# Performance work log

Hardware: AMD Instinct MI355X
Metric: run time of the kernel (lower is better)

The kernel has to match this reference:

```python
import jax, jax.numpy as jnp
import numpy as np

NUM_HEADS = 12

def get_rel_pos(q_size, k_size, rel_pos):
    # q_size == k_size here; relative index = i - j + (k_size - 1)
    idx = jnp.arange(q_size)[:, None] - jnp.arange(k_size)[None, :] + (k_size - 1)
    return rel_pos[idx]  # (q_size, k_size, head_dim)


def setup_inputs() -> dict:
    key = jax.random.key(0)
    ks = jax.random.split(key, 7)
    B, H, W, C = 1, 64, 64, 768
    return {
        "x": jax.random.normal(ks[0], (B, H, W, C), jnp.float32),
        "w_qkv": jax.random.normal(ks[1], (C, 3 * C), jnp.float32) * 0.02,
        "b_qkv": jnp.zeros((3 * C,), jnp.float32),
        "w_o": jax.random.normal(ks[2], (C, C), jnp.float32) * 0.02,
        "b_o": jnp.zeros((C,), jnp.float32),
        "rel_pos_h": jax.random.normal(ks[3], (2 * H - 1, C // NUM_HEADS), jnp.float32) * 0.02,
        "rel_pos_w": jax.random.normal(ks[4], (2 * W - 1, C // NUM_HEADS), jnp.float32) * 0.02,
    }


def reference(x, w_qkv, b_qkv, w_o, b_o, rel_pos_h, rel_pos_w):
    B, H, W, C = x.shape
    NH = NUM_HEADS
    HD = C // NH
    scale = HD ** -0.5  # 0.125

    qkv = x @ w_qkv + b_qkv                                   # (B,H,W,3C)
    qkv = qkv.reshape(B, H * W, 3, NH, HD)
    qkv = jnp.transpose(qkv, (2, 0, 3, 1, 4)).reshape(3, B * NH, H * W, HD)
    q, k, v = qkv[0], qkv[1], qkv[2]                          # (B*NH, HW, HD)

    Rh = get_rel_pos(H, H, rel_pos_h)                         # (H,H,HD)
    Rw = get_rel_pos(W, W, rel_pos_w)                         # (W,W,HD)
    qr = q.reshape(B * NH, H, W, HD)
    rel_h = jnp.einsum('bhwc,hkc->bhwk', qr, Rh)              # (B*NH,H,W,H)
    rel_w = jnp.einsum('bhwc,wkc->bhwk', qr, Rw)              # (B*NH,H,W,W)

    attn = jnp.einsum('bmd,bnd->bmn', q, k) * scale           # (B*NH,HW,HW)
    attn = attn.reshape(B * NH, H, W, H, W)
    attn = attn + rel_h[:, :, :, :, None] + rel_w[:, :, :, None, :]
    attn = attn.reshape(B * NH, H * W, H * W)

    p = jax.nn.softmax(attn, axis=-1)
    o = jnp.einsum('bmn,bnd->bmd', p, v)                      # (B*NH,HW,HD)
    o = o.reshape(B, NH, H * W, HD)
    o = jnp.transpose(o, (0, 2, 1, 3)).reshape(B, H, W, C)    # heads concat in channel dim
    return o @ w_o + b_o
```

## Files before the change

kernel.cpp:

```cpp
#include <hip/hip_runtime.h>

#define DEVI __device__ __forceinline__
typedef unsigned short u16;
typedef unsigned int u32;
typedef __attribute__((ext_vector_type(4))) float f4v;
typedef __attribute__((ext_vector_type(8))) short bf8v;
typedef __attribute__((ext_vector_type(4))) u32  u32x4;
typedef __attribute__((ext_vector_type(2))) u32  u32x2;
typedef __attribute__((ext_vector_type(4))) u16  u16x4;

#define AS1 __attribute__((address_space(1)))
#define AS3 __attribute__((address_space(3)))

DEVI u16 f2bf(float x){ union{float f;u32 u;} c{x}; u32 r=(c.u+0x7FFFu+((c.u>>16)&1u))>>16; return (u16)r; }
DEVI float bf2f(u16 b){ union{u32 u;float f;} c{(u32)b<<16}; return c.f; }
DEVI f4v mfma32(bf8v a, bf8v b, f4v c){ return __builtin_amdgcn_mfma_f32_16x16x32_bf16(a,b,c,0,0,0); }
DEVI unsigned lds_off(const void* p){ return (unsigned)(unsigned long)(AS3 const void*)p; }
DEVI void glds16(const void* g, void* l){
  __builtin_amdgcn_global_load_lds((AS1 void*)g, (AS3 void*)l, 16, 0, 0);
}

static constexpr int NH = 12, HW = 4096, D = 64, C = 768;
static constexpr float LOG2E = 1.44269504f;

__global__ void qa_convx(const float* __restrict__ x, u16* __restrict__ xb, int n4){
  int i = blockIdx.x*256 + threadIdx.x;
  if(i >= n4) return;
  f4v v = ((const f4v*)x)[i];
  u16x4 o; for(int j=0;j<4;j++) o[j] = f2bf(v[j]);
  ((u16x4*)xb)[i] = o;
}

__global__ void qa_transp(const float* __restrict__ in, u16* __restrict__ out, int R, int Cc, int scale_k){
  __shared__ float tl[32][33];
  int t = threadIdx.x;
  int r0 = blockIdx.y*32, c0 = blockIdx.x*32;
  int tr = t>>3, tc = (t&7)*4;
  f4v v = *(const f4v*)&in[(r0+tr)*Cc + c0 + tc];
  for(int j=0;j<4;j++) tl[tr][tc+j] = v[j];
  __syncthreads();
  int oc = t>>3, orr = (t&7)*4;
  float sc = (scale_k && (c0+oc) >= 768 && (c0+oc) < 1536) ? 0.125f*LOG2E : 1.0f;
  u16x4 o; for(int j=0;j<4;j++) o[j] = f2bf(tl[orr+j][oc]*sc);
  *(u16x4*)&out[(c0+oc)*R + r0 + orr] = o;
}

__global__ __launch_bounds__(256,2) void qa_gemm_qkv(
    const u16* __restrict__ A, const u16* __restrict__ Bt, const float* __restrict__ bias,
    u16* __restrict__ qb, u16* __restrict__ kb, u16* __restrict__ vb){
  __shared__ u16 Al[128*32], Bl[128*32];
  const int t = threadIdx.x, lane = t&63, w = t>>6, c16 = lane&15, h4 = lane>>4;
  const int m0 = blockIdx.y*128, n0 = blockIdx.x*128;
  const int wr = w>>1, wc = w&1;
  f4v acc[4][4];
  for(int nt=0;nt<4;nt++){
    f4v bv;
    for(int r=0;r<4;r++){
      int col = n0 + wc*64 + nt*16 + 4*h4 + r;
      float b = bias[col];
      bv[r] = (col >= 768 && col < 1536) ? b*0.125f*LOG2E : b;
    }
    for(int mt=0;mt<4;mt++) acc[mt][nt] = bv;
  }
  for(int k0 = 0; k0 < 768; k0 += 32){
    __syncthreads();
    for(int i=0;i<2;i++){
      int off = i*4096 + w*1024 + lane*16;
      int row = off>>6, kk = (off&63)>>1;
      glds16(A  + (size_t)(m0+row)*768 + k0 + kk, (u16*)Al + i*2048 + w*512);
      glds16(Bt + (size_t)(n0+row)*768 + k0 + kk, (u16*)Bl + i*2048 + w*512);
    }
    __syncthreads();
    bf8v a[4], b[4];
    for(int mt=0;mt<4;mt++) a[mt] = *(const bf8v*)&Al[(wr*64+mt*16+c16)*32 + h4*8];
    for(int nt=0;nt<4;nt++) b[nt] = *(const bf8v*)&Bl[(wc*64+nt*16+c16)*32 + h4*8];
    for(int mt=0;mt<4;mt++) for(int nt=0;nt<4;nt++) acc[mt][nt] = mfma32(b[nt], a[mt], acc[mt][nt]);
  }
  for(int mt=0;mt<4;mt++){
    int row = m0 + wr*64 + mt*16 + c16;
    for(int nt=0;nt<4;nt++){
      int col0 = n0 + wc*64 + nt*16 + 4*h4;
      int which = col0/768, head = (col0>>6)%12, d0 = col0&63;
      u16* dst = which==0 ? qb : (which==1 ? kb : vb);
      u32x2 pk;
      asm("v_cvt_pk_bf16_f32 %0, %1, %2" : "=v"(pk[0]) : "v"(acc[mt][nt][0]), "v"(acc[mt][nt][1]));
      asm("v_cvt_pk_bf16_f32 %0, %1, %2" : "=v"(pk[1]) : "v"(acc[mt][nt][2]), "v"(acc[mt][nt][3]));
      *(u32x2*)&dst[((size_t)(head<<12)+row)*64 + d0] = pk;
    }
  }
}

__global__ __launch_bounds__(256) void qa_rel(
    const u16* __restrict__ qbuf, const float* __restrict__ rph, const float* __restrict__ rpw,
    u16* __restrict__ RHt, u16* __restrict__ RW){
  const int t = threadIdx.x, lane = t&63, w = t>>6, c16 = lane&15, h4 = lane>>4;
  const int qh = blockIdx.x, head = blockIdx.y;
  __shared__ u16 ql[64*72], hl[64*72], wl[128*72];
  {
    int row = t>>2, d0 = (t&3)*16;
    const u16* src = qbuf + ((size_t)(head<<12)+(qh<<6)+row)*64 + d0;
    *(u32x4*)&ql[row*72+d0]   = *(const u32x4*)src;
    *(u32x4*)&ql[row*72+d0+8] = *(const u32x4*)(src+8);
    for(int j=0;j<16;j++) hl[row*72+d0+j] = f2bf(rph[(qh+row)*64 + d0 + j]);
    int rw_r = t>>1, rd0 = (t&1)*32;
    for(int j=0;j<32;j++) wl[rw_r*72+rd0+j] = (rw_r<127) ? f2bf(rpw[rw_r*64+rd0+j]) : (u16)0;
  }
  __syncthreads();
  if(w < 2){
    bf8v a[2][2]; f4v acc[2][4] = {};
    for(int mt=0;mt<2;mt++) for(int ch=0;ch<2;ch++)
      a[mt][ch] = *(const bf8v*)&ql[(w*32+mt*16+c16)*72 + ch*32 + h4*8];
    for(int nt=0;nt<4;nt++) for(int ch=0;ch<2;ch++){
      bf8v b = *(const bf8v*)&hl[(nt*16+c16)*72 + ch*32 + h4*8];
      for(int mt=0;mt<2;mt++) acc[mt][nt] = mfma32(a[mt][ch], b, acc[mt][nt]);
    }
    for(int mt=0;mt<2;mt++) for(int nt=0;nt<4;nt++) for(int r=0;r<4;r++){
      int qw = w*32+mt*16+4*h4+r, c = nt*16+c16, kh = 63 - c;
      RHt[((size_t)(head*64+qh)*64+kh)*64 + qw] = f2bf(acc[mt][nt][r]*LOG2E);
    }
  } else {
    bf8v a[2][2]; f4v acc[2][8] = {};
    for(int mt=0;mt<2;mt++) for(int ch=0;ch<2;ch++)
      a[mt][ch] = *(const bf8v*)&ql[((w-2)*32+mt*16+c16)*72 + ch*32 + h4*8];
    for(int nt=0;nt<8;nt++) for(int ch=0;ch<2;ch++){
      bf8v b = *(const bf8v*)&wl[(nt*16+c16)*72 + ch*32 + h4*8];
      for(int mt=0;mt<2;mt++) acc[mt][nt] = mfma32(a[mt][ch], b, acc[mt][nt]);
    }
    for(int mt=0;mt<2;mt++) for(int nt=0;nt<8;nt++) for(int r=0;r<4;r++){
      int qw = (w-2)*32+mt*16+4*h4+r, c = nt*16+c16, kw = qw + 63 - c;
      if((unsigned)kw < 64u) RW[((size_t)(head*64+qh)*64+qw)*64 + kw] = f2bf(acc[mt][nt][r]*LOG2E);
    }
  }
}

__global__ __launch_bounds__(256,3) void qa_attn(
    const u16* __restrict__ qb, const u16* __restrict__ kb, const u16* __restrict__ vb,
    const u16* __restrict__ RHt, const u16* __restrict__ RW,
    u16* __restrict__ Op, float* __restrict__ Ps){
  __shared__ u16 Kl[2][4096];
  __shared__ u16 Vl[2][4096];
  __shared__ u16 RHl[4096];
  const int t = threadIdx.x, lane = t&63, w = t>>6, c16 = lane&15, h4 = lane>>4;
  const int bid = blockIdx.x;
  const int g = (bid&7)*96 + (bid>>3);
  const int s = g&1, u = g>>1;
  const int head = u>>5, qblk = u&31;
  const int B0 = qblk*128;
  const int qhl = w>>1;

  for(int i=0;i<2;i++){
    const u16* rhsrc = RHt + (((size_t)(head*64 + qblk*2 + i))*64 + s*32)*64;
    glds16(rhsrc + t*8, (u16*)RHl + i*2048 + w*512);
  }

  int koff[2], voff[2];
  for(int i=0;i<2;i++){
    int uu = i*256 + t;
    koff[i] = (uu ^ ((uu>>3)&7))*8;
    int key = ((uu>>1)&3) | (((uu>>3)&15)<<2);
    int d0  = ((uu&1)<<3) | (((uu>>7)&3)<<4);
    voff[i] = key*64 + d0;
  }
  const u16* kg = kb + (size_t)head*262144 + (size_t)s*131072;
  const u16* vg = vb + (size_t)head*262144 + (size_t)s*131072;
  const u16* kp = kg; const u16* vp = vg;
  for(int i=0;i<2;i++){
    glds16(kp + koff[i], (u16*)Kl[0] + (i*256 + w*64)*8);
    glds16(vp + voff[i], (u16*)Vl[0] + (i*256 + w*64)*8);
  }
  kp += 4096; vp += 4096;

  bf8v qa[2][2];
  for(int qc=0;qc<2;qc++){
    const u16* qsrc = qb + ((size_t)head*4096 + B0 + w*32 + qc*16 + c16)*64;
    qa[qc][0] = *(const bf8v*)(qsrc + h4*8);
    qa[qc][1] = *(const bf8v*)(qsrc + 32 + h4*8);
  }
  float rw[4][2][4];
  for(int nt=0;nt<2*2;nt++);
  for(int nt=0;nt<4;nt++) for(int qc=0;qc<2;qc++) for(int r=0;r<4;r++){
    int qw = (w&1)*32 + qc*16 + c16, kw = nt*16 + 4*h4 + r;
    rw[nt][qc][r] = bf2f(RW[(((size_t)(head*64 + qblk*2 + qhl))*64 + qw)*64 + kw]);
  }

  f4v oacc[4][2] = {}; f4v psv[2] = {};
  unsigned vcur = lds_off(Vl) + lane*8;
  const int kq0 = (h4*16) ^ ((c16&7)<<4);
  const int kq1 = (h4*16 + 64) ^ ((c16&7)<<4);
  const int kA  = c16*128;

  for(int it=0; it<32; it++){
    if(it == 31){ kp = kg; vp = vg; }
    {
      u16* Kn = (u16*)Kl[(it+1)&1]; u16* Vn = (u16*)Vl[(it+1)&1];
      for(int i=0;i<2;i++){
        glds16(kp + koff[i], Kn + (i*256 + w*64)*8);
        glds16(vp + voff[i], Vn + (i*256 + w*64)*8);
      }
    }
    kp += 4096; vp += 4096;
    asm volatile("s_waitcnt vmcnt(4)\n\ts_barrier" ::: "memory");

    const char* Kc = (const char*)Kl + (it&1)*8192;
    float rh0 = bf2f(RHl[qhl*2048 + it*64 + (w&1)*32 + c16]);
    float rh1 = bf2f(RHl[qhl*2048 + it*64 + (w&1)*32 + 16 + c16]);
    f4v p[4][2];
    #pragma unroll
    for(int nt=0;nt<4;nt++){
      bf8v k0 = *(const bf8v*)(Kc + kA + nt*2048 + kq0);
      bf8v k1 = *(const bf8v*)(Kc + kA + nt*2048 + kq1);
      #pragma unroll
      for(int qc=0;qc<2;qc++){
        f4v sv;
        float rh = qc ? rh1 : rh0;
        for(int r=0;r<4;r++) sv[r] = rh + rw[nt][qc][r];
        __builtin_amdgcn_s_setprio(1);
        sv = mfma32(k0, qa[qc][0], sv);
        sv = mfma32(k1, qa[qc][1], sv);
        __builtin_amdgcn_s_setprio(0);
        f4v pe;
        for(int r=0;r<4;r++) pe[r] = __builtin_amdgcn_exp2f(sv[r]);
        p[nt][qc] = pe;
        psv[qc] += pe;
      }
    }
    union U8 { u32 w[4]; bf8v v; };
    U8 pb[2][2];
    #pragma unroll
    for(int half=0;half<2;half++)
      #pragma unroll
      for(int qc=0;qc<2;qc++)
        #pragma unroll
        for(int i=0;i<4;i++){
          int nt = half*2 + (i>>1), r0 = (i&1)*2;
          asm("v_cvt_pk_bf16_f32 %0, %1, %2"
              : "=v"(pb[half][qc].w[i]) : "v"(p[nt][qc][r0]), "v"(p[nt][qc][r0+1]));
        }
    #pragma unroll
    for(int dt=0;dt<4;dt++){
      unsigned long t00,t01,t10,t11;
      asm volatile(
        "ds_read_b64_tr_b16 %0, %4 offset:%c5\n\t"
        "ds_read_b64_tr_b16 %1, %4 offset:%c6\n\t"
        "ds_read_b64_tr_b16 %2, %4 offset:%c7\n\t"
        "ds_read_b64_tr_b16 %3, %4 offset:%c8\n\t"
        "s_waitcnt lgkmcnt(0)"
        : "=&v"(t00), "=&v"(t01), "=&v"(t10), "=&v"(t11)
        : "v"(vcur), "i"(dt*2048), "i"(dt*2048+512), "i"(dt*2048+1024), "i"(dt*2048+1536)
        : "memory");
      union { struct{ unsigned long a,b; } q; bf8v v; } v01, v23;
      v01.q.a = t00; v01.q.b = t01; v23.q.a = t10; v23.q.b = t11;
      __builtin_amdgcn_s_setprio(1);
      #pragma unroll
      for(int qc=0;qc<2;qc++){
        oacc[dt][qc] = mfma32(v01.v, pb[0][qc].v, oacc[dt][qc]);
        oacc[dt][qc] = mfma32(v23.v, pb[1][qc].v, oacc[dt][qc]);
      }
      __builtin_amdgcn_s_setprio(0);
    }
    asm volatile("s_waitcnt lgkmcnt(0)\n\ts_barrier" ::: "memory");
    vcur ^= 8192;
  }
  asm volatile("s_waitcnt vmcnt(0)" ::: "memory");

  #pragma unroll
  for(int qc=0;qc<2;qc++){
    float v = psv[qc][0]+psv[qc][1]+psv[qc][2]+psv[qc][3];
    v += __shfl_xor(v, 16); v += __shfl_xor(v, 32);
    const int qrow_l = w*32 + qc*16 + c16;
    if(h4 == 0) Ps[((size_t)u*2 + s)*128 + qrow_l] = v;
    const size_t obase = (((size_t)u*2 + s)*128 + qrow_l)*64;
    #pragma unroll
    for(int dt=0;dt<4;dt++){
      u32x2 pk;
      asm("v_cvt_pk_bf16_f32 %0, %1, %2" : "=v"(pk[0]) : "v"(oacc[dt][qc][0]), "v"(oacc[dt][qc][1]));
      asm("v_cvt_pk_bf16_f32 %0, %1, %2" : "=v"(pk[1]) : "v"(oacc[dt][qc][2]), "v"(oacc[dt][qc][3]));
      *(u32x2*)&Op[obase + dt*16 + 4*h4] = pk;
    }
  }
}

__global__ __launch_bounds__(256) void qa_reduce(
    const u16* __restrict__ Op, const float* __restrict__ Ps, u16* __restrict__ ob){
  const int u = blockIdx.x, t = threadIdx.x;
  const int head = u>>5, qblk = u&31;
  const int d0 = (t&15)*4;
  const size_t b0 = (size_t)u*2*128, b1 = b0 + 128;
  #pragma unroll
  for(int qq=0;qq<8;qq++){
    int qr = (t>>4) + qq*16;
    float inv = 1.0f / (Ps[b0 + qr] + Ps[b1 + qr]);
    u16x4 a = *(const u16x4*)&Op[(b0 + qr)*64 + d0];
    u16x4 b = *(const u16x4*)&Op[(b1 + qr)*64 + d0];
    u16x4 o;
    for(int j=0;j<4;j++) o[j] = f2bf((bf2f(a[j]) + bf2f(b[j]))*inv);
    *(u16x4*)&ob[(size_t)(qblk*128 + qr)*768 + head*64 + d0] = o;
  }
}

__global__ __launch_bounds__(256,2) void qa_gemm_out(
    const u16* __restrict__ A, const u16* __restrict__ Bt, const float* __restrict__ bias,
    float* __restrict__ out){
  __shared__ u16 Al[128*32], Bl[128*32];
  const int t = threadIdx.x, lane = t&63, w = t>>6, c16 = lane&15, h4 = lane>>4;
  const int m0 = blockIdx.y*128, n0 = blockIdx.x*128;
  const int wr = w>>1, wc = w&1;
  f4v acc[4][4];
  for(int nt=0;nt<4;nt++){
    f4v bv = *(const f4v*)&bias[n0 + wc*64 + nt*16 + 4*h4];
    for(int mt=0;mt<4;mt++) acc[mt][nt] = bv;
  }
  for(int k0 = 0; k0 < 768; k0 += 32){
    __syncthreads();
    for(int i=0;i<2;i++){
      int off = i*4096 + w*1024 + lane*16;
      int row = off>>6, kk = (off&63)>>1;
      glds16(A  + (size_t)(m0+row)*768 + k0 + kk, (u16*)Al + i*2048 + w*512);
      glds16(Bt + (size_t)(n0+row)*768 + k0 + kk, (u16*)Bl + i*2048 + w*512);
    }
    __syncthreads();
    bf8v a[4], b[4];
    for(int mt=0;mt<4;mt++) a[mt] = *(const bf8v*)&Al[(wr*64+mt*16+c16)*32 + h4*8];
    for(int nt=0;nt<4;nt++) b[nt] = *(const bf8v*)&Bl[(wc*64+nt*16+c16)*32 + h4*8];
    for(int mt=0;mt<4;mt++) for(int nt=0;nt<4;nt++) acc[mt][nt] = mfma32(b[nt], a[mt], acc[mt][nt]);
  }
  for(int mt=0;mt<4;mt++){
    int row = m0 + wr*64 + mt*16 + c16;
    for(int nt=0;nt<4;nt++){
      int col0 = n0 + wc*64 + nt*16 + 4*h4;
      *(f4v*)&out[(size_t)row*768 + col0] = acc[mt][nt];
    }
  }
}

extern "C" void kernel_launch(void* const* d_in, const int* in_sizes, int n_in,
                              void* d_out, int out_size, void* d_ws, size_t ws_size,
                              hipStream_t stream){
  const float* x    = (const float*)d_in[0];
  const float* wqkv = (const float*)d_in[1];
  const float* bqkv = (const float*)d_in[2];
  const float* wo   = (const float*)d_in[3];
  const float* bo   = (const float*)d_in[4];
  const float* rph  = (const float*)d_in[5];
  const float* rpw  = (const float*)d_in[6];
  float* out = (float*)d_out;

  size_t off = 0;
  auto alloc = [&](size_t bytes){ void* p = (char*)d_ws + off; off += (bytes + 255) & ~(size_t)255; return p; };
  u16* x_bf   = (u16*)alloc((size_t)HW*C*2);
  u16* wqkv_t = (u16*)alloc((size_t)2304*768*2);
  u16* wo_t   = (u16*)alloc((size_t)768*768*2);
  u16* q_buf  = (u16*)alloc((size_t)NH*HW*D*2);
  u16* k_buf  = (u16*)alloc((size_t)NH*HW*D*2);
  u16* v_buf  = (u16*)alloc((size_t)NH*HW*D*2);
  u16* rh_buf = (u16*)alloc((size_t)NH*64*64*64*2);
  u16* rw_buf = (u16*)alloc((size_t)NH*64*64*64*2);
  u16* o_buf  = (u16*)alloc((size_t)HW*C*2);
  u16* op_buf = (u16*)alloc((size_t)384*2*128*64*2);
  float* ps_buf = (float*)alloc((size_t)384*2*128*4);

  int n4 = HW*C/4;
  qa_convx<<<(n4+255)/256, 256, 0, stream>>>(x, x_bf, n4);
  qa_transp<<<dim3(2304/32, 768/32), 256, 0, stream>>>(wqkv, wqkv_t, 768, 2304, 1);
  qa_transp<<<dim3(768/32, 768/32),  256, 0, stream>>>(wo,   wo_t,   768, 768, 0);
  qa_gemm_qkv<<<dim3(2304/128, HW/128), 256, 0, stream>>>(x_bf, wqkv_t, bqkv, q_buf, k_buf, v_buf);
  qa_rel<<<dim3(64, NH), 256, 0, stream>>>(q_buf, rph, rpw, rh_buf, rw_buf);
  qa_attn<<<768, 256, 0, stream>>>(q_buf, k_buf, v_buf, rh_buf, rw_buf, op_buf, ps_buf);
  qa_reduce<<<384, 256, 0, stream>>>(op_buf, ps_buf, o_buf);
  qa_gemm_out<<<dim3(768/128, HW/128), 256, 0, stream>>>(o_buf, wo_t, bo, out);
}
```

Before: 144.1 us.

## Double-buffer GEMM LDS loads, compute softmax row sums via MFMA, vectorize rel-pos conversion

Both projection GEMMs now keep two LDS stages and issue the next K-tile's global-to-LDS loads before the current tile's MFMAs, replacing the two per-iteration __syncthreads with one barrier plus a vmcnt wait. The attention loop is unrolled by two with compile-time buffer indices and moves its barrier to the top of each iteration. The per-row exp sum now comes from an MFMA against a vector of ones instead of VALU adds and cross-lane shuffles. The rel-pos table conversion uses vector loads and packed bf16 converts. The row sum is now accumulated from bf16-rounded probabilities, which slightly changes numerics, and a single barrier per step relies on the vmcnt ordering being correct.

```diff
diff --git a/kernel.cpp b/kernel.cpp
--- a/kernel.cpp
+++ b/kernel.cpp
@@ -45,10 +45,27 @@
   *(u16x4*)&out[(c0+oc)*R + r0 + orr] = o;
 }
 
+#define GEMM_STAGE(K0, CUR) \
+  for(int i=0;i<2;i++){ \
+    glds16(A  + (size_t)(m0+srow[i])*768 + (K0) + skk[i], (u16*)Al[CUR] + i*2048 + w*512); \
+    glds16(Bt + (size_t)(n0+srow[i])*768 + (K0) + skk[i], (u16*)Bl[CUR] + i*2048 + w*512); }
+
+#define GEMM_STEP(KIDX, CUR) { \
+  asm volatile("s_barrier" ::: "memory"); \
+  if((KIDX) < 23){ GEMM_STAGE(((KIDX)+1)*32, (CUR)^1); \
+    asm volatile("s_waitcnt vmcnt(4)" ::: "memory"); \
+  } else { asm volatile("s_waitcnt vmcnt(0)" ::: "memory"); } \
+  bf8v a[4], b[4]; \
+  for(int mt=0;mt<4;mt++) a[mt] = *(const bf8v*)&Al[CUR][(wr*64+mt*16+c16)*32 + h4*8]; \
+  for(int nt=0;nt<4;nt++) b[nt] = *(const bf8v*)&Bl[CUR][(wc*64+nt*16+c16)*32 + h4*8]; \
+  __builtin_amdgcn_s_setprio(1); \
+  for(int mt=0;mt<4;mt++) for(int nt=0;nt<4;nt++) acc[mt][nt] = mfma32(b[nt], a[mt], acc[mt][nt]); \
+  __builtin_amdgcn_s_setprio(0); }
+
 __global__ __launch_bounds__(256,2) void qa_gemm_qkv(
     const u16* __restrict__ A, const u16* __restrict__ Bt, const float* __restrict__ bias,
     u16* __restrict__ qb, u16* __restrict__ kb, u16* __restrict__ vb){
-  __shared__ u16 Al[128*32], Bl[128*32];
+  __shared__ u16 Al[2][4096], Bl[2][4096];
   const int t = threadIdx.x, lane = t&63, w = t>>6, c16 = lane&15, h4 = lane>>4;
   const int m0 = blockIdx.y*128, n0 = blockIdx.x*128;
   const int wr = w>>1, wc = w&1;
@@ -62,20 +79,13 @@
     }
     for(int mt=0;mt<4;mt++) acc[mt][nt] = bv;
   }
-  for(int k0 = 0; k0 < 768; k0 += 32){
-    __syncthreads();
-    for(int i=0;i<2;i++){
-      int off = i*4096 + w*1024 + lane*16;
-      int row = off>>6, kk = (off&63)>>1;
-      glds16(A  + (size_t)(m0+row)*768 + k0 + kk, (u16*)Al + i*2048 + w*512);
-      glds16(Bt + (size_t)(n0+row)*768 + k0 + kk, (u16*)Bl + i*2048 + w*512);
-    }
-    __syncthreads();
-    bf8v a[4], b[4];
-    for(int mt=0;mt<4;mt++) a[mt] = *(const bf8v*)&Al[(wr*64+mt*16+c16)*32 + h4*8];
-    for(int nt=0;nt<4;nt++) b[nt] = *(const bf8v*)&Bl[(wc*64+nt*16+c16)*32 + h4*8];
-    for(int mt=0;mt<4;mt++) for(int nt=0;nt<4;nt++) acc[mt][nt] = mfma32(b[nt], a[mt], acc[mt][nt]);
-  }
+  int srow[2], skk[2];
+  for(int i=0;i<2;i++){
+    int off = i*4096 + w*1024 + lane*16;
+    srow[i] = off>>6; skk[i] = (off&63)>>1;
+  }
+  GEMM_STAGE(0, 0);
+  for(int p=0;p<12;p++){ GEMM_STEP(2*p, 0); GEMM_STEP(2*p+1, 1); }
   for(int mt=0;mt<4;mt++){
     int row = m0 + wr*64 + mt*16 + c16;
     for(int nt=0;nt<4;nt++){
@@ -101,9 +111,25 @@
     const u16* src = qbuf + ((size_t)(head<<12)+(qh<<6)+row)*64 + d0;
     *(u32x4*)&ql[row*72+d0]   = *(const u32x4*)src;
     *(u32x4*)&ql[row*72+d0+8] = *(const u32x4*)(src+8);
-    for(int j=0;j<16;j++) hl[row*72+d0+j] = f2bf(rph[(qh+row)*64 + d0 + j]);
+    for(int j=0;j<16;j+=4){
+      f4v v = *(const f4v*)&rph[(qh+row)*64 + d0 + j];
+      u32x2 pk;
+      asm("v_cvt_pk_bf16_f32 %0, %1, %2" : "=v"(pk[0]) : "v"(v[0]), "v"(v[1]));
+      asm("v_cvt_pk_bf16_f32 %0, %1, %2" : "=v"(pk[1]) : "v"(v[2]), "v"(v[3]));
+      *(u32x2*)&hl[row*72+d0+j] = pk;
+    }
     int rw_r = t>>1, rd0 = (t&1)*32;
-    for(int j=0;j<32;j++) wl[rw_r*72+rd0+j] = (rw_r<127) ? f2bf(rpw[rw_r*64+rd0+j]) : (u16)0;
+    if(rw_r < 127){
+      for(int j=0;j<32;j+=4){
+        f4v v = *(const f4v*)&rpw[rw_r*64+rd0+j];
+        u32x2 pk;
+        asm("v_cvt_pk_bf16_f32 %0, %1, %2" : "=v"(pk[0]) : "v"(v[0]), "v"(v[1]));
+        asm("v_cvt_pk_bf16_f32 %0, %1, %2" : "=v"(pk[1]) : "v"(v[2]), "v"(v[3]));
+        *(u32x2*)&wl[rw_r*72+rd0+j] = pk;
+      }
+    } else {
+      for(int j=0;j<32;j+=4) *(u32x2*)&wl[rw_r*72+rd0+j] = (u32x2){0u,0u};
+    }
   }
   __syncthreads();
   if(w < 2){
@@ -132,6 +158,71 @@
     }
   }
 }
+
+#define AITER(IT, CUR) { \
+    asm volatile("s_barrier" ::: "memory"); \
+    if((IT) == 31){ kp = kg; vp = vg; } \
+    { u16* Kn = (u16*)Kl[(CUR)^1]; u16* Vn = (u16*)Vl[(CUR)^1]; \
+      for(int i=0;i<2;i++){ \
+        glds16(kp + koff[i], Kn + (i*256 + w*64)*8); \
+        glds16(vp + voff[i], Vn + (i*256 + w*64)*8); } } \
+    kp += 4096; vp += 4096; \
+    asm volatile("s_waitcnt vmcnt(4)" ::: "memory"); \
+    const char* Kc = (const char*)Kl[CUR]; \
+    float rh0 = bf2f(RHl[qhl*2048 + (IT)*64 + (w&1)*32 + c16]); \
+    float rh1 = bf2f(RHl[qhl*2048 + (IT)*64 + (w&1)*32 + 16 + c16]); \
+    f4v p[4][2]; \
+    _Pragma("unroll") \
+    for(int nt=0;nt<4;nt++){ \
+      bf8v k0 = *(const bf8v*)(Kc + kA + nt*2048 + kq0); \
+      bf8v k1 = *(const bf8v*)(Kc + kA + nt*2048 + kq1); \
+      _Pragma("unroll") \
+      for(int qc=0;qc<2;qc++){ \
+        f4v sv; float rh = qc ? rh1 : rh0; \
+        for(int r=0;r<4;r++) sv[r] = rh + rw[nt][qc][r]; \
+        __builtin_amdgcn_s_setprio(1); \
+        sv = mfma32(k0, qa[qc][0], sv); \
+        sv = mfma32(k1, qa[qc][1], sv); \
+        __builtin_amdgcn_s_setprio(0); \
+        f4v pe; \
+        for(int r=0;r<4;r++) pe[r] = __builtin_amdgcn_exp2f(sv[r]); \
+        p[nt][qc] = pe; } } \
+    union U8 { u32 wd[4]; bf8v v; }; \
+    U8 pb[2][2]; \
+    _Pragma("unroll") \
+    for(int half=0;half<2;half++) \
+      for(int qc=0;qc<2;qc++) \
+        for(int i=0;i<4;i++){ \
+          int nt = half*2 + (i>>1), r0 = (i&1)*2; \
+          asm("v_cvt_pk_bf16_f32 %0, %1, %2" \
+              : "=v"(pb[half][qc].wd[i]) : "v"(p[nt][qc][r0]), "v"(p[nt][qc][r0+1])); } \
+    _Pragma("unroll") \
+    for(int qc=0;qc<2;qc++){ \
+      psacc[qc] = mfma32(onesv, pb[0][qc].v, psacc[qc]); \
+      psacc[qc] = mfma32(onesv, pb[1][qc].v, psacc[qc]); } \
+    unsigned vcur = vbase + (CUR)*8192; \
+    _Pragma("unroll") \
+    for(int dt=0;dt<4;dt++){ \
+      unsigned long t00,t01,t10,t11; \
+      asm volatile( \
+        "ds_read_b64_tr_b16 %0, %4 offset:%c5\n\t" \
+        "ds_read_b64_tr_b16 %1, %4 offset:%c6\n\t" \
+        "ds_read_b64_tr_b16 %2, %4 offset:%c7\n\t" \
+        "ds_read_b64_tr_b16 %3, %4 offset:%c8\n\t" \
+        "s_waitcnt lgkmcnt(0)" \
+        : "=&v"(t00), "=&v"(t01), "=&v"(t10), "=&v"(t11) \
+        : "v"(vcur), "i"((dt)*2048), "i"((dt)*2048+512), "i"((dt)*2048+1024), "i"((dt)*2048+1536) \
+        : "memory"); \
+      union PV { struct{ unsigned long a,b; } q; bf8v v; }; \
+      PV v01, v23; \
+      v01.q.a = t00; v01.q.b = t01; v23.q.a = t10; v23.q.b = t11; \
+      __builtin_amdgcn_s_setprio(1); \
+      _Pragma("unroll") \
+      for(int qc=0;qc<2;qc++){ \
+        oacc[dt][qc] = mfma32(v01.v, pb[0][qc].v, oacc[dt][qc]); \
+        oacc[dt][qc] = mfma32(v23.v, pb[1][qc].v, oacc[dt][qc]); } \
+      __builtin_amdgcn_s_setprio(0); } \
+  }
 
 __global__ __launch_bounds__(256,3) void qa_attn(
     const u16* __restrict__ qb, const u16* __restrict__ kb, const u16* __restrict__ vb,
@@ -152,7 +243,6 @@
     const u16* rhsrc = RHt + (((size_t)(head*64 + qblk*2 + i))*64 + s*32)*64;
     glds16(rhsrc + t*8, (u16*)RHl + i*2048 + w*512);
   }
-
   int koff[2], voff[2];
   for(int i=0;i<2;i++){
     int uu = i*256 + t;
@@ -177,96 +267,27 @@
     qa[qc][1] = *(const bf8v*)(qsrc + 32 + h4*8);
   }
   float rw[4][2][4];
-  for(int nt=0;nt<2*2;nt++);
   for(int nt=0;nt<4;nt++) for(int qc=0;qc<2;qc++) for(int r=0;r<4;r++){
     int qw = (w&1)*32 + qc*16 + c16, kw = nt*16 + 4*h4 + r;
     rw[nt][qc][r] = bf2f(RW[(((size_t)(head*64 + qblk*2 + qhl))*64 + qw)*64 + kw]);
   }
-
-  f4v oacc[4][2] = {}; f4v psv[2] = {};
-  unsigned vcur = lds_off(Vl) + lane*8;
+  bf8v onesv; for(int j=0;j<8;j++) onesv[j] = (short)0x3F80;
+
+  f4v oacc[4][2] = {}; f4v psacc[2] = {};
+  const unsigned vbase = lds_off(Vl) + lane*8;
   const int kq0 = (h4*16) ^ ((c16&7)<<4);
   const int kq1 = (h4*16 + 64) ^ ((c16&7)<<4);
   const int kA  = c16*128;
 
-  for(int it=0; it<32; it++){
-    if(it == 31){ kp = kg; vp = vg; }
-    {
-      u16* Kn = (u16*)Kl[(it+1)&1]; u16* Vn = (u16*)Vl[(it+1)&1];
-      for(int i=0;i<2;i++){
-        glds16(kp + koff[i], Kn + (i*256 + w*64)*8);
-        glds16(vp + voff[i], Vn + (i*256 + w*64)*8);
-      }
-    }
-    kp += 4096; vp += 4096;
-    asm volatile("s_waitcnt vmcnt(4)\n\ts_barrier" ::: "memory");
-
-    const char* Kc = (const char*)Kl + (it&1)*8192;
-    float rh0 = bf2f(RHl[qhl*2048 + it*64 + (w&1)*32 + c16]);
-    float rh1 = bf2f(RHl[qhl*2048 + it*64 + (w&1)*32 + 16 + c16]);
-    f4v p[4][2];
-    #pragma unroll
-    for(int nt=0;nt<4;nt++){
-      bf8v k0 = *(const bf8v*)(Kc + kA + nt*2048 + kq0);
-      bf8v k1 = *(const bf8v*)(Kc + kA + nt*2048 + kq1);
-      #pragma unroll
-      for(int qc=0;qc<2;qc++){
-        f4v sv;
-        float rh = qc ? rh1 : rh0;
-        for(int r=0;r<4;r++) sv[r] = rh + rw[nt][qc][r];
-        __builtin_amdgcn_s_setprio(1);
-        sv = mfma32(k0, qa[qc][0], sv);
-        sv = mfma32(k1, qa[qc][1], sv);
-        __builtin_amdgcn_s_setprio(0);
-        f4v pe;
-        for(int r=0;r<4;r++) pe[r] = __builtin_amdgcn_exp2f(sv[r]);
-        p[nt][qc] = pe;
-        psv[qc] += pe;
-      }
-    }
-    union U8 { u32 w[4]; bf8v v; };
-    U8 pb[2][2];
-    #pragma unroll
-    for(int half=0;half<2;half++)
-      #pragma unroll
-      for(int qc=0;qc<2;qc++)
-        #pragma unroll
-        for(int i=0;i<4;i++){
-          int nt = half*2 + (i>>1), r0 = (i&1)*2;
-          asm("v_cvt_pk_bf16_f32 %0, %1, %2"
-              : "=v"(pb[half][qc].w[i]) : "v"(p[nt][qc][r0]), "v"(p[nt][qc][r0+1]));
-        }
-    #pragma unroll
-    for(int dt=0;dt<4;dt++){
-      unsigned long t00,t01,t10,t11;
-      asm volatile(
-        "ds_read_b64_tr_b16 %0, %4 offset:%c5\n\t"
-        "ds_read_b64_tr_b16 %1, %4 offset:%c6\n\t"
-        "ds_read_b64_tr_b16 %2, %4 offset:%c7\n\t"
-        "ds_read_b64_tr_b16 %3, %4 offset:%c8\n\t"
-        "s_waitcnt lgkmcnt(0)"
-        : "=&v"(t00), "=&v"(t01), "=&v"(t10), "=&v"(t11)
-        : "v"(vcur), "i"(dt*2048), "i"(dt*2048+512), "i"(dt*2048+1024), "i"(dt*2048+1536)
-        : "memory");
-      union { struct{ unsigned long a,b; } q; bf8v v; } v01, v23;
-      v01.q.a = t00; v01.q.b = t01; v23.q.a = t10; v23.q.b = t11;
-      __builtin_amdgcn_s_setprio(1);
-      #pragma unroll
-      for(int qc=0;qc<2;qc++){
-        oacc[dt][qc] = mfma32(v01.v, pb[0][qc].v, oacc[dt][qc]);
-        oacc[dt][qc] = mfma32(v23.v, pb[1][qc].v, oacc[dt][qc]);
-      }
-      __builtin_amdgcn_s_setprio(0);
-    }
-    asm volatile("s_waitcnt lgkmcnt(0)\n\ts_barrier" ::: "memory");
-    vcur ^= 8192;
+  for(int itp=0; itp<16; itp++){
+    AITER(2*itp, 0);
+    AITER(2*itp+1, 1);
   }
   asm volatile("s_waitcnt vmcnt(0)" ::: "memory");
 
   #pragma unroll
   for(int qc=0;qc<2;qc++){
-    float v = psv[qc][0]+psv[qc][1]+psv[qc][2]+psv[qc][3];
-    v += __shfl_xor(v, 16); v += __shfl_xor(v, 32);
+    float v = psacc[qc][0];
     const int qrow_l = w*32 + qc*16 + c16;
     if(h4 == 0) Ps[((size_t)u*2 + s)*128 + qrow_l] = v;
     const size_t obase = (((size_t)u*2 + s)*128 + qrow_l)*64;
@@ -301,7 +322,7 @@
 __global__ __launch_bounds__(256,2) void qa_gemm_out(
     const u16* __restrict__ A, const u16* __restrict__ Bt, const float* __restrict__ bias,
     float* __restrict__ out){
-  __shared__ u16 Al[128*32], Bl[128*32];
+  __shared__ u16 Al[2][4096], Bl[2][4096];
   const int t = threadIdx.x, lane = t&63, w = t>>6, c16 = lane&15, h4 = lane>>4;
   const int m0 = blockIdx.y*128, n0 = blockIdx.x*128;
   const int wr = w>>1, wc = w&1;
@@ -310,20 +331,13 @@
     f4v bv = *(const f4v*)&bias[n0 + wc*64 + nt*16 + 4*h4];
     for(int mt=0;mt<4;mt++) acc[mt][nt] = bv;
   }
-  for(int k0 = 0; k0 < 768; k0 += 32){
-    __syncthreads();
-    for(int i=0;i<2;i++){
-      int off = i*4096 + w*1024 + lane*16;
-      int row = off>>6, kk = (off&63)>>1;
-      glds16(A  + (size_t)(m0+row)*768 + k0 + kk, (u16*)Al + i*2048 + w*512);
-      glds16(Bt + (size_t)(n0+row)*768 + k0 + kk, (u16*)Bl + i*2048 + w*512);
-    }
-    __syncthreads();
-    bf8v a[4], b[4];
-    for(int mt=0;mt<4;mt++) a[mt] = *(const bf8v*)&Al[(wr*64+mt*16+c16)*32 + h4*8];
-    for(int nt=0;nt<4;nt++) b[nt] = *(const bf8v*)&Bl[(wc*64+nt*16+c16)*32 + h4*8];
-    for(int mt=0;mt<4;mt++) for(int nt=0;nt<4;nt++) acc[mt][nt] = mfma32(b[nt], a[mt], acc[mt][nt]);
-  }
+  int srow[2], skk[2];
+  for(int i=0;i<2;i++){
+    int off = i*4096 + w*1024 + lane*16;
+    srow[i] = off>>6; skk[i] = (off&63)>>1;
+  }
+  GEMM_STAGE(0, 0);
+  for(int p=0;p<12;p++){ GEMM_STEP(2*p, 0); GEMM_STEP(2*p+1, 1); }
   for(int mt=0;mt<4;mt++){
     int row = m0 + wr*64 + mt*16 + c16;
     for(int nt=0;nt<4;nt++){
```

After: 138.8 us. -3.7%, faster.
